# Performance work log

Hardware: AMD Instinct MI355X
Metric: run time of the kernel (lower is better)

## Reference

```python
import jax, jax.numpy as jnp
import numpy as np

B, T, E, H, V = 64, 160, 512, 1024, 32000


def setup_inputs() -> dict:
    key = jax.random.key(0)
    ks = jax.random.split(key, 8)
    s = 1.0 / np.sqrt(H).astype(np.float32)
    return {
        "contexts": jax.random.randint(ks[0], (B, T), 0, V),
        "responses": jax.random.randint(ks[1], (B, T), 0, V),
        "emb": jax.random.normal(ks[2], (V, E), jnp.float32) * 0.02,
        "Wih": jax.random.uniform(ks[3], (4 * H, E), jnp.float32, -s, s),
        "Whh": jax.random.uniform(ks[4], (4 * H, H), jnp.float32, -s, s),
        "bih": jax.random.uniform(ks[5], (4 * H,), jnp.float32, -s, s),
        "bhh": jax.random.uniform(ks[6], (4 * H,), jnp.float32, -s, s),
        "M": jax.random.normal(ks[7], (H, H), jnp.float32),
    }


def _lstm_final_h(tokens, emb, Wih, Whh, bih, bhh):
    """Single-layer LSTM (PyTorch gate order i,f,g,o); returns final hidden state [B,H]."""
    x = emb[tokens]                      # [B, T, E]
    b = bih + bhh                        # [4H]
    hdim = Whh.shape[1]

    def step(carry, xt):
        h, c = carry
        gates = xt @ Wih.T + h @ Whh.T + b          # [B, 4H]
        i, f, g, o = jnp.split(gates, 4, axis=-1)
        c = jax.nn.sigmoid(f) * c + jax.nn.sigmoid(i) * jnp.tanh(g)
        h = jax.nn.sigmoid(o) * jnp.tanh(c)
        return (h, c), None

    h0 = jnp.zeros((tokens.shape[0], hdim), x.dtype)
    (h, _), _ = jax.lax.scan(step, (h0, h0), jnp.swapaxes(x, 0, 1))  # scan over time
    return h


def reference(contexts, responses, emb, Wih, Whh, bih, bhh, M):
    ch = _lstm_final_h(contexts, emb, Wih, Whh, bih, bhh)   # [B, H]
    rh = _lstm_final_h(responses, emb, Wih, Whh, bih, bhh)  # [B, H]
    # batched bilinear: sigmoid(diag(C @ M @ R^T)) -- replaces the per-example Python loop
    return jax.nn.sigmoid(jnp.einsum('bi,ij,bj->b', ch, M, rh))
```

## Files before the change

### kernel.cpp

```cpp
#include <hip/hip_runtime.h>
#include <math.h>


#define BB 64
#define TT 160
#define EE 512
#define HH 1024
#define G4 4096
#define ROWS 128
#define NB 256

typedef unsigned short u16;
typedef unsigned int u32;
typedef __attribute__((ext_vector_type(8))) __bf16 bf16x8;
typedef __attribute__((ext_vector_type(8))) short short8;
typedef __attribute__((ext_vector_type(4))) short short4v;
typedef __attribute__((ext_vector_type(4))) float f32x4;
typedef __attribute__((ext_vector_type(4))) u32 u32x4;

__device__ __forceinline__ u16 f2b(float f) {
    unsigned u = __float_as_uint(f);
    u = u + 0x7fffu + ((u >> 16) & 1u);
    return (u16)(u >> 16);
}
__device__ __forceinline__ float b2f(u16 s) { return __uint_as_float(((unsigned)s) << 16); }

__device__ __forceinline__ f32x4 mfma16(short8 a, short8 b, f32x4 c) {
    return __builtin_amdgcn_mfma_f32_16x16x32_bf16(
        __builtin_bit_cast(bf16x8, a), __builtin_bit_cast(bf16x8, b), c, 0, 0, 0);
}

__device__ __forceinline__ void g2l16(const void* gsrc, void* ldst) {
    __builtin_amdgcn_global_load_lds(
        (const __attribute__((address_space(1))) u32*)gsrc,
        (__attribute__((address_space(3))) u32*)ldst, 16, 0, 0);
}

__global__ __launch_bounds__(256) void cvt_kernel(const float* __restrict__ in,
                                                  u16* __restrict__ out, int n4) {
    int i = blockIdx.x * 256 + threadIdx.x;
    if (i < n4) {
        f32x4 v = *(const f32x4*)(in + (size_t)i * 4);
        short4v o;
        o.x = (short)f2b(v.x); o.y = (short)f2b(v.y);
        o.z = (short)f2b(v.z); o.w = (short)f2b(v.w);
        *(short4v*)(out + (size_t)i * 4) = o;
    }
}

__global__ __launch_bounds__(256) void pre_gemm2(
    const int* __restrict__ ctx, const int* __restrict__ rsp,
    const u16* __restrict__ embb, const u16* __restrict__ Wihb,
    const float* __restrict__ bih, const float* __restrict__ bhh,
    u16* __restrict__ xg)
{
    __shared__ __align__(16) u16 As[2][128][64];
    __shared__ __align__(16) u16 Ws[2][128][64];
    __shared__ int toks[128];
    const int tid = threadIdx.x;
    const int n0 = blockIdx.x * 128;
    const int t  = blockIdx.y;

    if (tid < 128) {
        int r = tid;
        toks[tid] = (r < BB) ? ctx[r * TT + t] : rsp[(r - BB) * TT + t];
    }
    __syncthreads();

    const u16* asrc[4]; const u16* bsrc[4];
    #pragma unroll
    for (int q = 0; q < 4; ++q) {
        int i = tid + q * 256;
        int row = i >> 3, c16 = i & 7;
        int scol = ((c16 ^ (row & 7)) * 8);
        asrc[q] = embb + (size_t)toks[row] * EE + scol;
        bsrc[q] = Wihb + (size_t)(n0 + row) * EE + scol;
    }

    const int lane = tid & 63, wave = tid >> 6;
    const int wr = (wave >> 1) * 64, wc = (wave & 1) * 64;
    const int l15 = lane & 15, l4 = lane >> 4;
    f32x4 acc[4][4] = {};

    #pragma unroll
    for (int q = 0; q < 4; ++q) {
        g2l16(asrc[q], (char*)&As[0][0][0] + (tid + q * 256) * 16);
        g2l16(bsrc[q], (char*)&Ws[0][0][0] + (tid + q * 256) * 16);
    }
    for (int it = 0; it < 8; ++it) {
        __syncthreads();
        if (it + 1 < 8) {
            int kk = (it + 1) * 64, bs = (it + 1) & 1;
            #pragma unroll
            for (int q = 0; q < 4; ++q) {
                g2l16(asrc[q] + kk, (char*)&As[bs][0][0] + (tid + q * 256) * 16);
                g2l16(bsrc[q] + kk, (char*)&Ws[bs][0][0] + (tid + q * 256) * 16);
            }
        }
        const int b = it & 1;
        #pragma unroll
        for (int ks = 0; ks < 2; ++ks) {
            int c16 = ks * 4 + l4;
            short8 a[4], w[4];
            #pragma unroll
            for (int mf = 0; mf < 4; ++mf) {
                int R = wr + mf * 16 + l15;
                a[mf] = *(const short8*)((const char*)&As[b][0][0] + R * 128 + ((c16 ^ (R & 7)) << 4));
            }
            #pragma unroll
            for (int nf = 0; nf < 4; ++nf) {
                int Nn = wc + nf * 16 + l15;
                w[nf] = *(const short8*)((const char*)&Ws[b][0][0] + Nn * 128 + ((c16 ^ (Nn & 7)) << 4));
            }
            #pragma unroll
            for (int mf = 0; mf < 4; ++mf)
                #pragma unroll
                for (int nf = 0; nf < 4; ++nf)
                    acc[mf][nf] = mfma16(a[mf], w[nf], acc[mf][nf]);
        }
    }

    u16* xp = xg + (size_t)t * ROWS * G4;
    #pragma unroll
    for (int nf = 0; nf < 4; ++nf) {
        int n = n0 + wc + nf * 16 + l15;
        float bias = bih[n] + bhh[n];
        #pragma unroll
        for (int mf = 0; mf < 4; ++mf)
            #pragma unroll
            for (int q = 0; q < 4; ++q) {
                int r = wr + mf * 16 + l4 * 4 + q;
                xp[(size_t)r * G4 + n] = f2b(acc[mf][nf][q] + bias);
            }
    }
}

__global__ __launch_bounds__(512) void lstm_persist3(
    const u16* __restrict__ Whhb, const u16* __restrict__ xg,
    u16* __restrict__ hbuf, u32* __restrict__ flags)
{
    __shared__ float G[2][2][32][33];

    const int tid = threadIdx.x;
    const int bx = blockIdx.x;
    const int cg = bx & 127, rg = bx >> 7;
    const int r0 = rg * 64, j0 = cg * 8;

    const int lane = tid & 63, wave = tid >> 6;
    const int rsub = wave >> 2;
    const int kh   = wave & 3;
    const int l15 = lane & 15, l4 = lane >> 4;

    short8 breg[2][8];
    #pragma unroll
    for (int nf = 0; nf < 2; ++nf) {
        int c = nf * 16 + l15;
        int n = (c >> 3) * HH + j0 + (c & 7);
        const u16* wp = Whhb + (size_t)n * HH + kh * 256 + l4 * 8;
        #pragma unroll
        for (int ks = 0; ks < 8; ++ks)
            breg[nf][ks] = *(const short8*)(wp + ks * 32);
    }

    const int ur = tid >> 2;
    const int uj = (tid & 3) * 2;
    float c0 = 0.f, c1 = 0.f;

    __syncthreads();

    for (int t = 0; t < TT; ++t) {
        const u16* hin = hbuf + (size_t)(t & 1) * ROWS * HH;
        u16* hout      = hbuf + (size_t)((t + 1) & 1) * ROWS * HH;

        const u16* abase = hin + (size_t)(r0 + rsub * 32 + l15) * HH + kh * 256 + l4 * 8;
        short8 a[2][8];
        #pragma unroll
        for (int half = 0; half < 2; ++half)
            #pragma unroll
            for (int ks = 0; ks < 8; ++ks)
                asm volatile("global_load_dwordx4 %0, %1, off sc0 sc1"
                             : "=v"(a[half][ks])
                             : "v"(abase + half * 16 * HH + ks * 32));

        u32 xv0, xv1, xv2, xv3;
        {
            const u16* xp = xg + ((size_t)t * ROWS + r0 + ur) * G4 + j0 + uj;
            asm volatile("global_load_dword %0, %1, off" : "=v"(xv0) : "v"(xp));
            asm volatile("global_load_dword %0, %1, off" : "=v"(xv1) : "v"(xp + HH));
            asm volatile("global_load_dword %0, %1, off" : "=v"(xv2) : "v"(xp + 2 * HH));
            asm volatile("global_load_dword %0, %1, off" : "=v"(xv3) : "v"(xp + 3 * HH));
        }
        asm volatile("s_waitcnt vmcnt(4)" ::: "memory");
        __builtin_amdgcn_sched_barrier(0);

        f32x4 acc[2][2] = {};
        #pragma unroll
        for (int ks = 0; ks < 8; ++ks) {
            acc[0][0] = mfma16(a[0][ks], breg[0][ks], acc[0][0]);
            acc[0][1] = mfma16(a[0][ks], breg[1][ks], acc[0][1]);
            acc[1][0] = mfma16(a[1][ks], breg[0][ks], acc[1][0]);
            acc[1][1] = mfma16(a[1][ks], breg[1][ks], acc[1][1]);
        }

        if (kh < 2) {
            #pragma unroll
            for (int mf = 0; mf < 2; ++mf)
                #pragma unroll
                for (int nf = 0; nf < 2; ++nf)
                    #pragma unroll
                    for (int q = 0; q < 4; ++q)
                        G[kh][rsub][mf * 16 + l4 * 4 + q][nf * 16 + l15] = acc[mf][nf][q];
        }
        __syncthreads();
        if (kh >= 2) {
            #pragma unroll
            for (int mf = 0; mf < 2; ++mf)
                #pragma unroll
                for (int nf = 0; nf < 2; ++nf)
                    #pragma unroll
                    for (int q = 0; q < 4; ++q)
                        G[kh - 2][rsub][mf * 16 + l4 * 4 + q][nf * 16 + l15] += acc[mf][nf][q];
        }
        __syncthreads();

        asm volatile("s_waitcnt vmcnt(0)" ::: "memory");
        __builtin_amdgcn_sched_barrier(0);
        if (tid < 256) {
            const int rs = ur >> 5, rl = ur & 31;
            float g0[4], g1[4];
            u32 xv[4] = {xv0, xv1, xv2, xv3};
            #pragma unroll
            for (int q = 0; q < 4; ++q) {
                float x0 = b2f((u16)(xv[q] & 0xffffu));
                float x1 = b2f((u16)(xv[q] >> 16));
                g0[q] = G[0][rs][rl][q * 8 + uj]     + G[1][rs][rl][q * 8 + uj]     + x0;
                g1[q] = G[0][rs][rl][q * 8 + uj + 1] + G[1][rs][rl][q * 8 + uj + 1] + x1;
            }
            float i0 = 1.f / (1.f + expf(-g0[0])), i1 = 1.f / (1.f + expf(-g1[0]));
            float f0 = 1.f / (1.f + expf(-g0[1])), f1 = 1.f / (1.f + expf(-g1[1]));
            float t0 = tanhf(g0[2]),               t1 = tanhf(g1[2]);
            float o0 = 1.f / (1.f + expf(-g0[3])), o1 = 1.f / (1.f + expf(-g1[3]));
            c0 = f0 * c0 + i0 * t0;
            c1 = f1 * c1 + i1 * t1;
            float h0 = o0 * tanhf(c0), h1 = o1 * tanhf(c1);
            u32 hp = (u32)f2b(h0) | ((u32)f2b(h1) << 16);
            u16* hptr = hout + (size_t)(r0 + ur) * HH + j0 + uj;
            asm volatile("global_store_dword %0, %1, off sc0 sc1"
                         :: "v"(hptr), "v"(hp) : "memory");
        }

        if (t < TT - 1) {
            asm volatile("s_waitcnt vmcnt(0)" ::: "memory");
            __syncthreads();
            const u32 target = (u32)(t + 1);
            if (tid == 0) {
                asm volatile("global_store_dword %0, %1, off sc0 sc1"
                             :: "v"(flags + bx), "v"(target) : "memory");
            }
            if (wave == 0) {
                const u32* fp = flags + rg * 128 + (lane & 31) * 4;
                int spins = 0;
                while (true) {
                    u32x4 fv;
                    asm volatile("global_load_dwordx4 %0, %1, off sc0 sc1"
                                 : "=v"(fv) : "v"(fp));
                    asm volatile("s_waitcnt vmcnt(0)" ::: "memory");
                    bool ok = (fv.x >= target) & (fv.y >= target) &
                              (fv.z >= target) & (fv.w >= target);
                    if (__all(ok)) break;
                    __builtin_amdgcn_s_sleep(2);
                    if (++spins > 4000000) break;
                }
            }
            __syncthreads();
            __builtin_amdgcn_sched_barrier(0);
        }
    }
}

template<int MODE>
__global__ __launch_bounds__(256) void step_fused(
    const int* __restrict__ ctx, const int* __restrict__ rsp,
    const u16* __restrict__ embb, const u16* __restrict__ Wihb,
    const u16* __restrict__ Whhb, const u16* __restrict__ xg,
    const float* __restrict__ bih, const float* __restrict__ bhh,
    const u16* __restrict__ hin, u16* __restrict__ hout,
    float* __restrict__ c_ws, int t)
{
    __shared__ __align__(16) u16 As[2][64][64];
    __shared__ __align__(16) u16 Ws[2][32][64];
    __shared__ float gs[64][32];
    __shared__ int toks[64];

    const int tid = threadIdx.x;
    const int cg = blockIdx.x & 127, rg = blockIdx.x >> 7;
    const int r0 = rg * 64, j0 = cg * 8;

    if (MODE == 1) {
        if (tid < 64) {
            int r = r0 + tid;
            toks[tid] = (r < BB) ? ctx[r * TT + t] : rsp[(r - BB) * TT + t];
        }
        __syncthreads();
    }

    const int arow0 = tid >> 3, c16a = tid & 7;
    const int arow1 = arow0 + 32;
    const int acol0 = ((c16a ^ (arow0 & 7)) * 8);
    const int acol1 = ((c16a ^ (arow1 & 7)) * 8);
    const u16* hA0 = hin + (size_t)(r0 + arow0) * HH + acol0;
    const u16* hA1 = hin + (size_t)(r0 + arow1) * HH + acol1;
    const u16* eA0 = nullptr; const u16* eA1 = nullptr;
    if (MODE == 1) {
        eA0 = embb + (size_t)toks[arow0] * EE + acol0;
        eA1 = embb + (size_t)toks[arow1] * EE + acol1;
    }
    const int nn = tid >> 3, c16b = tid & 7;
    const int bcol = ((c16b ^ (nn & 7)) * 8);
    const int wrow = (nn >> 3) * HH + j0 + (nn & 7);
    const u16* wHh = Whhb + (size_t)wrow * HH + bcol;
    const u16* wIh = (MODE == 1) ? (Wihb + (size_t)wrow * EE + bcol) : nullptr;

    const int NK = (MODE == 1) ? 24 : 16;

    auto stage = [&](int bs, int it) {
        int kk = it * 64;
        const u16 *s0, *s1, *sw;
        if (MODE == 1 && kk < EE) {
            s0 = eA0 + kk; s1 = eA1 + kk; sw = wIh + kk;
        } else {
            int khh = (MODE == 1) ? kk - EE : kk;
            s0 = hA0 + khh; s1 = hA1 + khh; sw = wHh + khh;
        }
        g2l16(s0, (char*)&As[bs][0][0] + tid * 16);
        g2l16(s1, (char*)&As[bs][0][0] + (tid + 256) * 16);
        g2l16(sw, (char*)&Ws[bs][0][0] + tid * 16);
    };

    const int lane = tid & 63, wave = tid >> 6;
    const int wr = wave * 16;
    const int l15 = lane & 15, l4 = lane >> 4;
    f32x4 acc[2] = {};

    stage(0, 0);
    for (int it = 0; it < NK; ++it) {
        __syncthreads();
        if (it + 1 < NK) stage((it + 1) & 1, it + 1);
        const int b = it & 1;
        #pragma unroll
        for (int ks = 0; ks < 2; ++ks) {
            int c16 = ks * 4 + l4;
            int R = wr + l15;
            short8 a = *(const short8*)((const char*)&As[b][0][0] + R * 128 + ((c16 ^ (R & 7)) << 4));
            #pragma unroll
            for (int nf = 0; nf < 2; ++nf) {
                int Nn = nf * 16 + l15;
                short8 w = *(const short8*)((const char*)&Ws[b][0][0] + Nn * 128 + ((c16 ^ (Nn & 7)) << 4));
                acc[nf] = mfma16(a, w, acc[nf]);
            }
        }
    }
    __syncthreads();
    #pragma unroll
    for (int nf = 0; nf < 2; ++nf)
        #pragma unroll
        for (int q = 0; q < 4; ++q)
            gs[wr + l4 * 4 + q][nf * 16 + l15] = acc[nf][q];
    __syncthreads();

    const int e = tid * 2;
    const int row = e >> 3, jj = e & 7;
    const int rglob = r0 + row;
    float g0[4], g1[4];
    #pragma unroll
    for (int g = 0; g < 4; ++g) { g0[g] = gs[row][g * 8 + jj]; g1[g] = gs[row][g * 8 + jj + 1]; }
    if (MODE == 2) {
        const u16* xp = xg + ((size_t)t * ROWS + rglob) * G4 + j0 + jj;
        #pragma unroll
        for (int g = 0; g < 4; ++g) { g0[g] += b2f(xp[g * HH]); g1[g] += b2f(xp[g * HH + 1]); }
    } else {
        #pragma unroll
        for (int g = 0; g < 4; ++g) {
            int n = g * HH + j0 + jj;
            g0[g] += bih[n] + bhh[n];
            g1[g] += bih[n + 1] + bhh[n + 1];
        }
    }
    size_t cidx = ((size_t)blockIdx.x * 64 + row) * 8 + jj;
    float c0 = c_ws[cidx], c1 = c_ws[cidx + 1];
    float i0 = 1.f / (1.f + expf(-g0[0])), i1 = 1.f / (1.f + expf(-g1[0]));
    float f0 = 1.f / (1.f + expf(-g0[1])), f1 = 1.f / (1.f + expf(-g1[1]));
    float t0 = tanhf(g0[2]),               t1 = tanhf(g1[2]);
    float o0 = 1.f / (1.f + expf(-g0[3])), o1 = 1.f / (1.f + expf(-g1[3]));
    float cn0 = f0 * c0 + i0 * t0;
    float cn1 = f1 * c1 + i1 * t1;
    c_ws[cidx] = cn0; c_ws[cidx + 1] = cn1;
    float h0 = o0 * tanhf(cn0), h1 = o1 * tanhf(cn1);
    unsigned hp = (unsigned)f2b(h0) | ((unsigned)f2b(h1) << 16);
    *(unsigned*)(hout + (size_t)rglob * HH + j0 + jj) = hp;
}

__global__ __launch_bounds__(256) void step_gemm_f32(
    const int* __restrict__ ctx, const int* __restrict__ rsp,
    const float* __restrict__ emb, const float* __restrict__ Wih, const float* __restrict__ Whh,
    const u16* __restrict__ hb, float* __restrict__ gates, int t)
{
    __shared__ __align__(16) u16 As[64][32];
    __shared__ __align__(16) u16 Ws[64][32];
    __shared__ int toks[64];
    const int tid = threadIdx.x;
    const int n0 = blockIdx.x * 64;
    const int r0 = blockIdx.y * 64;
    const int part = blockIdx.z;
    if (tid < 64) {
        int r = r0 + tid;
        toks[tid] = (r < BB) ? ctx[r * TT + t] : rsp[(r - BB) * TT + t];
    }
    __syncthreads();
    const int lane = tid & 63, wave = tid >> 6;
    const int wr = (wave >> 1) * 32, wc = (wave & 1) * 32;
    const int l15 = lane & 15, l4 = lane >> 4;
    f32x4 acc[2][2] = {};
    const int kstart = part * 768;
    const int srow = tid >> 2;
    const int sseg = (tid & 3) * 8;
    for (int it = 0; it < 24; ++it) {
        const int kg = kstart + it * 32;
        const int kk = kg + sseg;
        if (kg < EE) {
            const float* s = emb + (size_t)toks[srow] * EE + kk;
            #pragma unroll
            for (int q = 0; q < 8; ++q) As[srow][sseg + q] = f2b(s[q]);
            const float* sw = Wih + (size_t)(n0 + srow) * EE + kk;
            #pragma unroll
            for (int q = 0; q < 8; ++q) Ws[srow][sseg + q] = f2b(sw[q]);
        } else {
            *(short8*)&As[srow][sseg] = *(const short8*)(hb + (size_t)(r0 + srow) * HH + (kk - EE));
            const float* sw = Whh + (size_t)(n0 + srow) * HH + (kk - EE);
            #pragma unroll
            for (int q = 0; q < 8; ++q) Ws[srow][sseg + q] = f2b(sw[q]);
        }
        __syncthreads();
        #pragma unroll
        for (int mf = 0; mf < 2; ++mf)
            #pragma unroll
            for (int nf = 0; nf < 2; ++nf)
                acc[mf][nf] = mfma16(*(const short8*)&As[wr + mf * 16 + l15][l4 * 8],
                                     *(const short8*)&Ws[wc + nf * 16 + l15][l4 * 8], acc[mf][nf]);
        __syncthreads();
    }
    float* gp = gates + (size_t)part * ROWS * G4;
    #pragma unroll
    for (int mf = 0; mf < 2; ++mf)
        #pragma unroll
        for (int nf = 0; nf < 2; ++nf)
            #pragma unroll
            for (int q = 0; q < 4; ++q) {
                int r = r0 + wr + mf * 16 + l4 * 4 + q;
                int n = n0 + wc + nf * 16 + l15;
                gp[(size_t)r * G4 + n] = acc[mf][nf][q];
            }
}

__global__ __launch_bounds__(256) void lstm_update0(
    const float* __restrict__ gates, const float* __restrict__ bih, const float* __restrict__ bhh,
    u16* __restrict__ hb, float* __restrict__ c)
{
    int idx = blockIdx.x * 256 + threadIdx.x;
    int r = idx >> 8;
    int jj = (idx & 255) * 4;
    const float* gp0 = gates + (size_t)r * G4;
    const float* gp1 = gates + (size_t)(ROWS + r) * G4;
    float gate[4][4];
    #pragma unroll
    for (int g = 0; g < 4; ++g) {
        int n = g * HH + jj;
        f32x4 a = *(const f32x4*)(gp0 + n);
        f32x4 b = *(const f32x4*)(gp1 + n);
        #pragma unroll
        for (int q = 0; q < 4; ++q) gate[g][q] = a[q] + b[q] + bih[n + q] + bhh[n + q];
    }
    int cidx = r * HH + jj;
    f32x4 cv = *(const f32x4*)(c + cidx);
    f32x4 cn; short4v hn;
    #pragma unroll
    for (int q = 0; q < 4; ++q) {
        float si = 1.f / (1.f + expf(-gate[0][q]));
        float sf = 1.f / (1.f + expf(-gate[1][q]));
        float tg = tanhf(gate[2][q]);
        float so = 1.f / (1.f + expf(-gate[3][q]));
        float cval = sf * cv[q] + si * tg;
        cn[q] = cval;
        ((short*)&hn)[q] = (short)f2b(so * tanhf(cval));
    }
    *(f32x4*)(c + cidx) = cn;
    *(short4v*)(hb + cidx) = hn;
}

__global__ __launch_bounds__(256) void bilinear(
    const u16* __restrict__ hb, const float* __restrict__ M, float* __restrict__ out)
{
    int b = blockIdx.x;
    __shared__ float chs[HH];
    __shared__ float red[256];
    const u16* ch = hb + (size_t)b * HH;
    const u16* rh = hb + (size_t)(BB + b) * HH;
    for (int i = threadIdx.x; i < HH; i += 256) chs[i] = b2f(ch[i]);
    __syncthreads();
    float vj[4] = {0.f, 0.f, 0.f, 0.f};
    for (int i = 0; i < HH; ++i) {
        float chi = chs[i];
        const float* Mr = M + (size_t)i * HH;
        #pragma unroll
        for (int q = 0; q < 4; ++q) vj[q] += chi * Mr[threadIdx.x + q * 256];
    }
    float acc = 0.f;
    #pragma unroll
    for (int q = 0; q < 4; ++q) acc += vj[q] * b2f(rh[threadIdx.x + q * 256]);
    red[threadIdx.x] = acc;
    __syncthreads();
    for (int s = 128; s > 0; s >>= 1) {
        if (threadIdx.x < s) red[threadIdx.x] += red[threadIdx.x + s];
        __syncthreads();
    }
    if (threadIdx.x == 0) out[b] = 1.0f / (1.0f + expf(-red[0]));
}

extern "C" void kernel_launch(void* const* d_in, const int* in_sizes, int n_in,
                              void* d_out, int out_size, void* d_ws, size_t ws_size,
                              hipStream_t stream) {
    const int*   ctx = (const int*)d_in[0];
    const int*   rsp = (const int*)d_in[1];
    const float* emb = (const float*)d_in[2];
    const float* Wih = (const float*)d_in[3];
    const float* Whh = (const float*)d_in[4];
    const float* bih = (const float*)d_in[5];
    const float* bhh = (const float*)d_in[6];
    const float* M   = (const float*)d_in[7];
    float* out = (float*)d_out;

    char* w = (char*)d_ws;
    u16*   hbuf  = (u16*)w;   w += (size_t)2 * ROWS * HH * 2;
    float* c_ws  = (float*)w; w += (size_t)ROWS * HH * 4;
    float* gates = (float*)w; w += (size_t)2 * ROWS * G4 * 4;
    u16*   embb  = (u16*)w;   w += (size_t)32000 * EE * 2;
    u16*   Wihb  = (u16*)w;   w += (size_t)G4 * EE * 2;
    u16*   Whhb  = (u16*)w;   w += (size_t)G4 * HH * 2;
    u32*   flags = (u32*)w;   w += 1024;
    size_t conv_need = (size_t)(w - (char*)d_ws);
    u16*   xg    = (u16*)w;   w += (size_t)TT * ROWS * G4 * 2;
    size_t xpre_need = (size_t)(w - (char*)d_ws);

    int mode = (ws_size >= xpre_need) ? 2 : (ws_size >= conv_need) ? 1 : 0;

    hipMemsetAsync(hbuf, 0, (size_t)2 * ROWS * HH * 2, stream);

    if (mode >= 1) {
        cvt_kernel<<<16000, 256, 0, stream>>>(emb, embb, 32000 * EE / 4);
        cvt_kernel<<<2048,  256, 0, stream>>>(Wih, Wihb, G4 * EE / 4);
        cvt_kernel<<<4096,  256, 0, stream>>>(Whh, Whhb, G4 * HH / 4);
    }

    if (mode == 2) {
        hipMemsetAsync(flags, 0, 1024, stream);
        pre_gemm2<<<dim3(G4 / 128, TT), 256, 0, stream>>>(ctx, rsp, embb, Wihb, bih, bhh, xg);
        lstm_persist3<<<NB, 512, 0, stream>>>(Whhb, xg, hbuf, flags);
        bilinear<<<BB, 256, 0, stream>>>(hbuf, M, out);
    } else if (mode == 1) {
        hipMemsetAsync(c_ws, 0, (size_t)ROWS * HH * 4, stream);
        for (int t = 0; t < TT; ++t) {
            const u16* hin = hbuf + (size_t)(t & 1) * ROWS * HH;
            u16* hout      = hbuf + (size_t)((t + 1) & 1) * ROWS * HH;
            step_fused<1><<<256, 256, 0, stream>>>(ctx, rsp, embb, Wihb, Whhb, xg,
                                                   bih, bhh, hin, hout, c_ws, t);
        }
        bilinear<<<BB, 256, 0, stream>>>(hbuf, M, out);
    } else {
        hipMemsetAsync(c_ws, 0, (size_t)ROWS * HH * 4, stream);
        u16* hb = hbuf;
        dim3 sg(G4 / 64, ROWS / 64, 2);
        for (int t = 0; t < TT; ++t) {
            step_gemm_f32<<<sg, 256, 0, stream>>>(ctx, rsp, emb, Wih, Whh, hb, gates, t);
            lstm_update0<<<128, 256, 0, stream>>>(gates, bih, bhh, hb, c_ws);
        }
        bilinear<<<BB, 256, 0, stream>>>(hb, M, out);
    }
}
```

Before: 2.078 ms.

## Repartition persistent LSTM kernel to 64 blocks with LDS-staged swizzled hidden state

The persistent recurrent kernel drops from 256 blocks of 8 hidden columns to 64 blocks of 32 columns. Each block stages its 64x1024 slice of h into LDS in two halves, using async global-to-LDS loads with an XOR swizzle, and all waves then read their A fragments from that copy. This is meant to cut redundant global reads of h and shrink the grid-wide flag barrier from 128 peers to 32 per row group. In exchange each block does four times the MFMA and gate work, and far fewer CUs share the per-step compute.

```diff
diff --git a/kernel.cpp b/kernel.cpp
--- a/kernel.cpp
+++ b/kernel.cpp
@@ -8,7 +8,7 @@
 #define HH 1024
 #define G4 4096
 #define ROWS 128
-#define NB 256
+#define NBLK 64
 
 typedef unsigned short u16;
 typedef unsigned int u32;
@@ -17,6 +17,7 @@
 typedef __attribute__((ext_vector_type(4))) short short4v;
 typedef __attribute__((ext_vector_type(4))) float f32x4;
 typedef __attribute__((ext_vector_type(4))) u32 u32x4;
+typedef __attribute__((ext_vector_type(2))) u32 u32x2;
 
 __device__ __forceinline__ u16 f2b(float f) {
     unsigned u = __float_as_uint(f);
@@ -34,6 +35,11 @@
     __builtin_amdgcn_global_load_lds(
         (const __attribute__((address_space(1))) u32*)gsrc,
         (__attribute__((address_space(3))) u32*)ldst, 16, 0, 0);
+}
+__device__ __forceinline__ void g2l16c(const void* gsrc, void* ldst) {
+    __builtin_amdgcn_global_load_lds(
+        (const __attribute__((address_space(1))) u32*)gsrc,
+        (__attribute__((address_space(3))) u32*)ldst, 16, 0, 17);
 }
 
 __global__ __launch_bounds__(256) void cvt_kernel(const float* __restrict__ in,
@@ -135,36 +141,36 @@
     }
 }
 
-__global__ __launch_bounds__(512) void lstm_persist3(
+__global__ __launch_bounds__(512, 2) void lstm_persist4(
     const u16* __restrict__ Whhb, const u16* __restrict__ xg,
     u16* __restrict__ hbuf, u32* __restrict__ flags)
 {
-    __shared__ float G[2][2][32][33];
+    __shared__ __align__(16) u16 Abuf[64][512];
+    __shared__ __align__(16) float G[2][64][132];
 
     const int tid = threadIdx.x;
     const int bx = blockIdx.x;
-    const int cg = bx & 127, rg = bx >> 7;
-    const int r0 = rg * 64, j0 = cg * 8;
-
-    const int lane = tid & 63, wave = tid >> 6;
-    const int rsub = wave >> 2;
-    const int kh   = wave & 3;
+    const int cg = bx & 31, rg = bx >> 5;
+    const int r0 = rg * 64, j0 = cg * 32;
+    const int lane = tid & 63, w = tid >> 6;
+    const int colt = w >> 2, q = w & 3;
     const int l15 = lane & 15, l4 = lane >> 4;
 
-    short8 breg[2][8];
-    #pragma unroll
-    for (int nf = 0; nf < 2; ++nf) {
-        int c = nf * 16 + l15;
-        int n = (c >> 3) * HH + j0 + (c & 7);
-        const u16* wp = Whhb + (size_t)n * HH + kh * 256 + l4 * 8;
-        #pragma unroll
-        for (int ks = 0; ks < 8; ++ks)
-            breg[nf][ks] = *(const short8*)(wp + ks * 32);
-    }
-
-    const int ur = tid >> 2;
-    const int uj = (tid & 3) * 2;
-    float c0 = 0.f, c1 = 0.f;
+    short8 breg[4][8];
+    #pragma unroll
+    for (int nt = 0; nt < 4; ++nt) {
+        int n = (colt * 2 + (nt >> 1)) * 1024 + j0 + (nt & 1) * 16 + l15;
+        const u16* wp = Whhb + (size_t)n * HH + l4 * 8;
+        #pragma unroll
+        for (int z = 0; z < 8; ++z) {
+            int kc = (z < 4) ? (q * 4 + z) : (16 + q * 4 + (z - 4));
+            breg[nt][z] = *(const short8*)(wp + kc * 32);
+        }
+    }
+
+    const int urow = tid >> 3;
+    const int jj4  = (tid & 7) * 4;
+    float cst[4] = {0.f, 0.f, 0.f, 0.f};
 
     __syncthreads();
 
@@ -172,93 +178,146 @@
         const u16* hin = hbuf + (size_t)(t & 1) * ROWS * HH;
         u16* hout      = hbuf + (size_t)((t + 1) & 1) * ROWS * HH;
 
-        const u16* abase = hin + (size_t)(r0 + rsub * 32 + l15) * HH + kh * 256 + l4 * 8;
-        short8 a[2][8];
-        #pragma unroll
-        for (int half = 0; half < 2; ++half)
-            #pragma unroll
-            for (int ks = 0; ks < 8; ++ks)
-                asm volatile("global_load_dwordx4 %0, %1, off sc0 sc1"
-                             : "=v"(a[half][ks])
-                             : "v"(abase + half * 16 * HH + ks * 32));
-
-        u32 xv0, xv1, xv2, xv3;
+        #pragma unroll
+        for (int j = 0; j < 8; ++j) {
+            int row = w * 8 + j;
+            const u16* src = hin + (size_t)(r0 + row) * HH + ((lane ^ j) * 8);
+            g2l16c(src, &Abuf[row][0]);
+        }
+        u32x2 xv[4];
         {
-            const u16* xp = xg + ((size_t)t * ROWS + r0 + ur) * G4 + j0 + uj;
-            asm volatile("global_load_dword %0, %1, off" : "=v"(xv0) : "v"(xp));
-            asm volatile("global_load_dword %0, %1, off" : "=v"(xv1) : "v"(xp + HH));
-            asm volatile("global_load_dword %0, %1, off" : "=v"(xv2) : "v"(xp + 2 * HH));
-            asm volatile("global_load_dword %0, %1, off" : "=v"(xv3) : "v"(xp + 3 * HH));
-        }
+            const u16* xp = xg + ((size_t)t * ROWS + r0 + urow) * G4 + j0 + jj4;
+            #pragma unroll
+            for (int g = 0; g < 4; ++g)
+                asm volatile("global_load_dwordx2 %0, %1, off"
+                             : "=v"(xv[g]) : "v"(xp + g * HH));
+        }
+
+        f32x4 acc[4][4] = {};
+
         asm volatile("s_waitcnt vmcnt(4)" ::: "memory");
         __builtin_amdgcn_sched_barrier(0);
-
-        f32x4 acc[2][2] = {};
-        #pragma unroll
-        for (int ks = 0; ks < 8; ++ks) {
-            acc[0][0] = mfma16(a[0][ks], breg[0][ks], acc[0][0]);
-            acc[0][1] = mfma16(a[0][ks], breg[1][ks], acc[0][1]);
-            acc[1][0] = mfma16(a[1][ks], breg[0][ks], acc[1][0]);
-            acc[1][1] = mfma16(a[1][ks], breg[1][ks], acc[1][1]);
-        }
-
-        if (kh < 2) {
-            #pragma unroll
-            for (int mf = 0; mf < 2; ++mf)
+        __builtin_amdgcn_s_barrier();
+        __builtin_amdgcn_sched_barrier(0);
+        #pragma unroll
+        for (int z4 = 0; z4 < 4; ++z4) {
+            const int kcl = q * 4 + z4;
+            short8 a[4];
+            #pragma unroll
+            for (int rt = 0; rt < 4; ++rt) {
+                int row = rt * 16 + l15;
+                int c16 = kcl * 4 + l4;
+                a[rt] = *(const short8*)((const char*)&Abuf[0][0] +
+                         row * 1024 + ((c16 ^ (l15 & 7)) << 4));
+            }
+            #pragma unroll
+            for (int rt = 0; rt < 4; ++rt)
                 #pragma unroll
-                for (int nf = 0; nf < 2; ++nf)
-                    #pragma unroll
-                    for (int q = 0; q < 4; ++q)
-                        G[kh][rsub][mf * 16 + l4 * 4 + q][nf * 16 + l15] = acc[mf][nf][q];
-        }
-        __syncthreads();
-        if (kh >= 2) {
-            #pragma unroll
-            for (int mf = 0; mf < 2; ++mf)
-                #pragma unroll
-                for (int nf = 0; nf < 2; ++nf)
-                    #pragma unroll
-                    for (int q = 0; q < 4; ++q)
-                        G[kh - 2][rsub][mf * 16 + l4 * 4 + q][nf * 16 + l15] += acc[mf][nf][q];
-        }
-        __syncthreads();
-
+                for (int nt = 0; nt < 4; ++nt)
+                    acc[rt][nt] = mfma16(a[rt], breg[nt][z4], acc[rt][nt]);
+        }
+        asm volatile("s_waitcnt lgkmcnt(0)" ::: "memory");
+        __builtin_amdgcn_s_barrier();
+        __builtin_amdgcn_sched_barrier(0);
+
+        #pragma unroll
+        for (int j = 0; j < 8; ++j) {
+            int row = w * 8 + j;
+            const u16* src = hin + (size_t)(r0 + row) * HH + 512 + ((lane ^ j) * 8);
+            g2l16c(src, &Abuf[row][0]);
+        }
         asm volatile("s_waitcnt vmcnt(0)" ::: "memory");
         __builtin_amdgcn_sched_barrier(0);
-        if (tid < 256) {
-            const int rs = ur >> 5, rl = ur & 31;
-            float g0[4], g1[4];
-            u32 xv[4] = {xv0, xv1, xv2, xv3};
-            #pragma unroll
-            for (int q = 0; q < 4; ++q) {
-                float x0 = b2f((u16)(xv[q] & 0xffffu));
-                float x1 = b2f((u16)(xv[q] >> 16));
-                g0[q] = G[0][rs][rl][q * 8 + uj]     + G[1][rs][rl][q * 8 + uj]     + x0;
-                g1[q] = G[0][rs][rl][q * 8 + uj + 1] + G[1][rs][rl][q * 8 + uj + 1] + x1;
-            }
-            float i0 = 1.f / (1.f + expf(-g0[0])), i1 = 1.f / (1.f + expf(-g1[0]));
-            float f0 = 1.f / (1.f + expf(-g0[1])), f1 = 1.f / (1.f + expf(-g1[1]));
-            float t0 = tanhf(g0[2]),               t1 = tanhf(g1[2]);
-            float o0 = 1.f / (1.f + expf(-g0[3])), o1 = 1.f / (1.f + expf(-g1[3]));
-            c0 = f0 * c0 + i0 * t0;
-            c1 = f1 * c1 + i1 * t1;
-            float h0 = o0 * tanhf(c0), h1 = o1 * tanhf(c1);
-            u32 hp = (u32)f2b(h0) | ((u32)f2b(h1) << 16);
-            u16* hptr = hout + (size_t)(r0 + ur) * HH + j0 + uj;
-            asm volatile("global_store_dword %0, %1, off sc0 sc1"
-                         :: "v"(hptr), "v"(hp) : "memory");
+        __builtin_amdgcn_s_barrier();
+        __builtin_amdgcn_sched_barrier(0);
+        #pragma unroll
+        for (int z4 = 0; z4 < 4; ++z4) {
+            const int kcl = q * 4 + z4;
+            short8 a[4];
+            #pragma unroll
+            for (int rt = 0; rt < 4; ++rt) {
+                int row = rt * 16 + l15;
+                int c16 = kcl * 4 + l4;
+                a[rt] = *(const short8*)((const char*)&Abuf[0][0] +
+                         row * 1024 + ((c16 ^ (l15 & 7)) << 4));
+            }
+            #pragma unroll
+            for (int rt = 0; rt < 4; ++rt)
+                #pragma unroll
+                for (int nt = 0; nt < 4; ++nt)
+                    acc[rt][nt] = mfma16(a[rt], breg[nt][4 + z4], acc[rt][nt]);
+        }
+
+        if (q < 2) {
+            #pragma unroll
+            for (int rt = 0; rt < 4; ++rt)
+                #pragma unroll
+                for (int nt = 0; nt < 4; ++nt) {
+                    int col = colt * 64 + nt * 16 + l15;
+                    int rowb = rt * 16 + l4 * 4;
+                    #pragma unroll
+                    for (int e = 0; e < 4; ++e)
+                        G[q][rowb + e][col] = acc[rt][nt][e];
+                }
+        }
+        asm volatile("s_waitcnt lgkmcnt(0)" ::: "memory");
+        __builtin_amdgcn_s_barrier();
+        __builtin_amdgcn_sched_barrier(0);
+        if (q >= 2) {
+            #pragma unroll
+            for (int rt = 0; rt < 4; ++rt)
+                #pragma unroll
+                for (int nt = 0; nt < 4; ++nt) {
+                    int col = colt * 64 + nt * 16 + l15;
+                    int rowb = rt * 16 + l4 * 4;
+                    #pragma unroll
+                    for (int e = 0; e < 4; ++e)
+                        G[q - 2][rowb + e][col] += acc[rt][nt][e];
+                }
+        }
+        asm volatile("s_waitcnt lgkmcnt(0)" ::: "memory");
+        __builtin_amdgcn_s_barrier();
+        __builtin_amdgcn_sched_barrier(0);
+
+        float gv[4][4];
+        #pragma unroll
+        for (int g = 0; g < 4; ++g) {
+            f32x4 a0 = *(const f32x4*)&G[0][urow][g * 32 + jj4];
+            f32x4 a1 = *(const f32x4*)&G[1][urow][g * 32 + jj4];
+            gv[g][0] = a0.x + a1.x + b2f((u16)(xv[g].x & 0xffffu));
+            gv[g][1] = a0.y + a1.y + b2f((u16)(xv[g].x >> 16));
+            gv[g][2] = a0.z + a1.z + b2f((u16)(xv[g].y & 0xffffu));
+            gv[g][3] = a0.w + a1.w + b2f((u16)(xv[g].y >> 16));
+        }
+        u16 hp[4];
+        #pragma unroll
+        for (int e = 0; e < 4; ++e) {
+            float ii = 1.f / (1.f + expf(-gv[0][e]));
+            float ff = 1.f / (1.f + expf(-gv[1][e]));
+            float gg = tanhf(gv[2][e]);
+            float oo = 1.f / (1.f + expf(-gv[3][e]));
+            cst[e] = ff * cst[e] + ii * gg;
+            hp[e] = f2b(oo * tanhf(cst[e]));
+        }
+        u32x2 hw;
+        hw.x = (u32)hp[0] | ((u32)hp[1] << 16);
+        hw.y = (u32)hp[2] | ((u32)hp[3] << 16);
+        {
+            u16* hpt = hout + (size_t)(r0 + urow) * HH + j0 + jj4;
+            asm volatile("global_store_dwordx2 %0, %1, off sc0 sc1"
+                         :: "v"(hpt), "v"(hw) : "memory");
         }
 
         if (t < TT - 1) {
             asm volatile("s_waitcnt vmcnt(0)" ::: "memory");
-            __syncthreads();
+            __builtin_amdgcn_s_barrier();
+            __builtin_amdgcn_sched_barrier(0);
             const u32 target = (u32)(t + 1);
-            if (tid == 0) {
+            if (tid == 0)
                 asm volatile("global_store_dword %0, %1, off sc0 sc1"
                              :: "v"(flags + bx), "v"(target) : "memory");
-            }
-            if (wave == 0) {
-                const u32* fp = flags + rg * 128 + (lane & 31) * 4;
+            if (w == 0) {
+                const u32* fp = flags + rg * 32 + (lane & 7) * 4;
                 int spins = 0;
                 while (true) {
                     u32x4 fv;
@@ -269,10 +328,10 @@
                               (fv.z >= target) & (fv.w >= target);
                     if (__all(ok)) break;
                     __builtin_amdgcn_s_sleep(2);
-                    if (++spins > 4000000) break;
+                    if (++spins > 2000000) break;
                 }
             }
-            __syncthreads();
+            __builtin_amdgcn_s_barrier();
             __builtin_amdgcn_sched_barrier(0);
         }
     }
@@ -396,8 +455,8 @@
     float cn1 = f1 * c1 + i1 * t1;
     c_ws[cidx] = cn0; c_ws[cidx + 1] = cn1;
     float h0 = o0 * tanhf(cn0), h1 = o1 * tanhf(cn1);
-    unsigned hp = (unsigned)f2b(h0) | ((unsigned)f2b(h1) << 16);
-    *(unsigned*)(hout + (size_t)rglob * HH + j0 + jj) = hp;
+    unsigned hpk = (unsigned)f2b(h0) | ((unsigned)f2b(h1) << 16);
+    *(unsigned*)(hout + (size_t)rglob * HH + j0 + jj) = hpk;
 }
 
 __global__ __launch_bounds__(256) void step_gemm_f32(
@@ -564,7 +623,7 @@
     if (mode == 2) {
         hipMemsetAsync(flags, 0, 1024, stream);
         pre_gemm2<<<dim3(G4 / 128, TT), 256, 0, stream>>>(ctx, rsp, embb, Wihb, bih, bhh, xg);
-        lstm_persist3<<<NB, 512, 0, stream>>>(Whhb, xg, hbuf, flags);
+        lstm_persist4<<<NBLK, 512, 0, stream>>>(Whhb, xg, hbuf, flags);
         bilinear<<<BB, 256, 0, stream>>>(hbuf, M, out);
     } else if (mode == 1) {
         hipMemsetAsync(c_ws, 0, (size_t)ROWS * HH * 4, stream);
```

New measurement: 2.005 ms. 1.04x faster.
